# Optimization experiments

Hardware: AMD Instinct MI355X
Metric: run time of the kernel (lower is better)

Reference implementation:

```python
import jax, jax.numpy as jnp
import numpy as np
import math

D_MODEL = 1024
N_HEADS = 16
HEAD_DIM = 64


def setup_inputs() -> dict:
    key = jax.random.key(0)
    k_x, k_q, k_k, k_v, k_o = jax.random.split(key, 5)
    lecun = jax.nn.initializers.lecun_normal()
    return {
        "x": jax.random.normal(k_x, (4, 2048, D_MODEL), dtype=jnp.float32),
        "W_q": lecun(k_q, (N_HEADS, D_MODEL, HEAD_DIM), jnp.float32),
        "W_k": lecun(k_k, (N_HEADS, D_MODEL, HEAD_DIM), jnp.float32),
        "W_v": lecun(k_v, (N_HEADS, D_MODEL, HEAD_DIM), jnp.float32),
        "W_o": lecun(k_o, (D_MODEL, D_MODEL), jnp.float32),
    }


def reference(x, W_q, W_k, W_v, W_o):
    # x: [b, l, e]; W_{q,k,v}: [h, e, d]; W_o: [e, e]
    q = jnp.einsum('ble,hed->bhld', x, W_q)
    k = jnp.einsum('ble,hed->bhld', x, W_k)
    v = jnp.einsum('ble,hed->bhld', x, W_v)
    scores = jnp.einsum('bhld,bhsd->bhls', q, k) / math.sqrt(HEAD_DIM)
    attn = jax.nn.softmax(scores, axis=-1)
    av = jnp.einsum('bhls,bhsd->bhld', attn, v)  # [b, h, l, d]
    b, h, l, d = av.shape
    concat = jnp.transpose(av, (0, 2, 1, 3)).reshape(b, l, h * d)
    out = jnp.einsum('ble,eo->blo', concat, W_o)
    return jnp.asarray(out, dtype=jnp.float32)
```

## Files before the change

### kernel.cpp

```cpp
#include <hip/hip_runtime.h>

#define BATCH 4
#define LSEQ  2048
#define DM    1024
#define NH    16
#define HD    64
#define NTOK  (BATCH * LSEQ)

typedef _Float16 f16x8 __attribute__((ext_vector_type(8)));
typedef _Float16 f16x4 __attribute__((ext_vector_type(4)));
typedef __fp16   hf16x2 __attribute__((ext_vector_type(2)));
typedef float    f32x4 __attribute__((ext_vector_type(4)));

typedef __attribute__((address_space(1))) const unsigned int GU32;
typedef __attribute__((address_space(3))) unsigned int LU32;

__device__ __forceinline__ void gload_lds16(const _Float16* g, _Float16* l)
{
    __builtin_amdgcn_global_load_lds(
        (GU32*)(unsigned long long)g,
        (LU32*)(unsigned int)(unsigned long long)l, 16, 0, 0);
}


__global__ __launch_bounds__(256) void cvt_kernel(const float* __restrict__ src,
                                                  _Float16* __restrict__ dst, int n4)
{
    int i = blockIdx.x * 256 + threadIdx.x;
    if (i >= n4) return;
    float4 v = ((const float4*)src)[i];
    f16x4 h;
    h[0] = (_Float16)v.x; h[1] = (_Float16)v.y; h[2] = (_Float16)v.z; h[3] = (_Float16)v.w;
    ((f16x4*)dst)[i] = h;
}

__global__ __launch_bounds__(256) void tconv3_kernel(
    const float* __restrict__ Wq, const float* __restrict__ Wk,
    const float* __restrict__ Wv, _Float16* __restrict__ dst)
{
    const int z = blockIdx.z;
    const int which = z >> 4, h = z & 15;
    const float* __restrict__ src =
        ((which == 0) ? Wq : (which == 1) ? Wk : Wv) + (size_t)h * DM * HD;
    _Float16* __restrict__ d = dst + (size_t)z * DM * HD;
    const int e0 = blockIdx.y * 64;
    __shared__ float Ls[64][65];
    const int t = threadIdx.x;
    #pragma unroll
    for (int j = 0; j < 4; ++j) {
        int cidx = t + j * 256;
        int row = cidx >> 4, col4 = (cidx & 15) * 4;
        float4 v = *(const float4*)&src[(size_t)(e0 + row) * HD + col4];
        Ls[row][col4] = v.x; Ls[row][col4+1] = v.y; Ls[row][col4+2] = v.z; Ls[row][col4+3] = v.w;
    }
    __syncthreads();
    const int dd = t & 63, sc = t >> 6;
    alignas(16) _Float16 tmp[16];
    #pragma unroll
    for (int i = 0; i < 16; ++i) tmp[i] = (_Float16)Ls[sc * 16 + i][dd];
    *(f16x8*)&d[(size_t)dd * DM + e0 + sc * 16]     = *(f16x8*)&tmp[0];
    *(f16x8*)&d[(size_t)dd * DM + e0 + sc * 16 + 8] = *(f16x8*)&tmp[8];
}

__global__ __launch_bounds__(256) void tconv_kernel(const float* __restrict__ src,
                                                    _Float16* __restrict__ dst, int E, int D)
{
    const int d0 = blockIdx.x * 64, e0 = blockIdx.y * 64;
    __shared__ float Ls[64][65];
    const int t = threadIdx.x;
    #pragma unroll
    for (int j = 0; j < 4; ++j) {
        int cidx = t + j * 256;
        int row = cidx >> 4, col4 = (cidx & 15) * 4;
        float4 v = *(const float4*)&src[(size_t)(e0 + row) * D + d0 + col4];
        Ls[row][col4] = v.x; Ls[row][col4+1] = v.y; Ls[row][col4+2] = v.z; Ls[row][col4+3] = v.w;
    }
    __syncthreads();
    const int dd = t & 63, sc = t >> 6;
    alignas(16) _Float16 tmp[16];
    #pragma unroll
    for (int i = 0; i < 16; ++i) tmp[i] = (_Float16)Ls[sc * 16 + i][dd];
    *(f16x8*)&dst[(size_t)(d0 + dd) * E + e0 + sc * 16]     = *(f16x8*)&tmp[0];
    *(f16x8*)&dst[(size_t)(d0 + dd) * E + e0 + sc * 16 + 8] = *(f16x8*)&tmp[8];
}

template<int MODE>
__global__ __launch_bounds__(256) void gemm_kernel(
    const _Float16* __restrict__ A, const _Float16* __restrict__ B,
    float* __restrict__ out32,
    _Float16* __restrict__ qo, _Float16* __restrict__ ko, _Float16* __restrict__ vto)
{
    const int n0 = blockIdx.x * 128, m0 = blockIdx.y * 128;
    __shared__ _Float16 As[128 * 64];
    __shared__ _Float16 Bs[128 * 64];
    const int t = threadIdx.x;
    const int lane = t & 63, w = t >> 6;
    const int quad = lane >> 4, c = lane & 15;
    const int wm = (w & 1) * 64, wn = (w >> 1) * 64;
    const int srow = lane >> 3;
    const int scol8 = ((lane & 7) ^ (lane >> 3)) * 8;

    const int colsw = (quad ^ (c & 7)) * 8;
    const _Float16* Ap0 = &As[(wm + c) * 64 + colsw];
    const _Float16* Ap1 = &As[(wm + c) * 64 + (colsw ^ 32)];
    const _Float16* Bp0 = &Bs[(wn + c) * 64 + colsw];
    const _Float16* Bp1 = &Bs[(wn + c) * 64 + (colsw ^ 32)];

    f32x4 acc[4][4];
    #pragma unroll
    for (int i = 0; i < 4; ++i)
        #pragma unroll
        for (int j = 0; j < 4; ++j) acc[i][j] = {0.f, 0.f, 0.f, 0.f};

    for (int e0 = 0; e0 < DM; e0 += 64) {
        __syncthreads();
        #pragma unroll
        for (int j = 0; j < 4; ++j) {
            int ch = w * 4 + j;
            gload_lds16(A + (size_t)(m0 + ch * 8 + srow) * DM + e0 + scol8, As + ch * 512);
            gload_lds16(B + (size_t)(n0 + ch * 8 + srow) * DM + e0 + scol8, Bs + ch * 512);
        }
        __syncthreads();
        #pragma unroll
        for (int kc = 0; kc < 2; ++kc) {
            const _Float16* Ap = kc ? Ap1 : Ap0;
            const _Float16* Bp = kc ? Bp1 : Bp0;
            f16x8 af[4], bf[4];
            #pragma unroll
            for (int mt = 0; mt < 4; ++mt) af[mt] = *(const f16x8*)(Ap + mt * 1024);
            #pragma unroll
            for (int nt = 0; nt < 4; ++nt) bf[nt] = *(const f16x8*)(Bp + nt * 1024);
            #pragma unroll
            for (int mt = 0; mt < 4; ++mt)
                #pragma unroll
                for (int nt = 0; nt < 4; ++nt)
                    acc[mt][nt] = __builtin_amdgcn_mfma_f32_16x16x32_f16(af[mt], bf[nt], acc[mt][nt], 0, 0, 0);
        }
    }

    if (MODE == 0) {
        #pragma unroll
        for (int mt = 0; mt < 4; ++mt)
            #pragma unroll
            for (int nt = 0; nt < 4; ++nt)
                #pragma unroll
                for (int r = 0; r < 4; ++r) {
                    int row = m0 + wm + mt * 16 + quad * 4 + r;
                    int col = n0 + wn + nt * 16 + c;
                    out32[(size_t)row * DM + col] = acc[mt][nt][r];
                }
    } else {
        const int mi = (n0 + wn) >> 6;
        const int which = mi >> 4, hh = mi & 15;
        if (which == 2) {
            #pragma unroll
            for (int mt = 0; mt < 4; ++mt) {
                int tok0 = m0 + wm + mt * 16 + quad * 4;
                int b = tok0 >> 11, l = tok0 & (LSEQ - 1);
                #pragma unroll
                for (int nt = 0; nt < 4; ++nt) {
                    int d = nt * 16 + c;
                    f16x4 pk;
                    pk[0] = (_Float16)acc[mt][nt][0];
                    pk[1] = (_Float16)acc[mt][nt][1];
                    pk[2] = (_Float16)acc[mt][nt][2];
                    pk[3] = (_Float16)acc[mt][nt][3];
                    *(f16x4*)&vto[((size_t)(b * NH + hh) * HD + d) * LSEQ + l] = pk;
                }
            }
        } else {
            _Float16* dst = (which == 0) ? qo : ko;
            const float vs = (which == 0) ? 0.18033688011112042f : 1.0f;
            #pragma unroll
            for (int mt = 0; mt < 4; ++mt)
                #pragma unroll
                for (int nt = 0; nt < 4; ++nt)
                    #pragma unroll
                    for (int r = 0; r < 4; ++r) {
                        int tok = m0 + wm + mt * 16 + quad * 4 + r;
                        int b = tok >> 11, l = tok & (LSEQ - 1);
                        int d = nt * 16 + c;
                        dst[((size_t)(b * NH + hh) * LSEQ + l) * HD + d] = (_Float16)(acc[mt][nt][r] * vs);
                    }
        }
    }
}

__global__ __launch_bounds__(256, 4) void attn_kernel(
    const _Float16* __restrict__ Qg, const _Float16* __restrict__ Kg,
    const _Float16* __restrict__ Vtg, _Float16* __restrict__ concat)
{
    const int bh = blockIdx.x;
    const int q0 = blockIdx.y * 128;
    const int b = bh >> 4, h = bh & (NH - 1);
    __shared__ _Float16 Ks[64 * 64];
    __shared__ _Float16 Vts[64 * 64];
    __shared__ _Float16 Ps[4][32][72];
    const int t = threadIdx.x;
    const int lane = t & 63, w = t >> 6;
    const int quad = lane >> 4, c = lane & 15;
    const int srow = lane >> 3;
    const int scol8 = ((lane & 7) ^ (lane >> 3)) * 8;

    const int colsw = (quad ^ (c & 7)) * 8;
    const _Float16* Kp0 = &Ks[c * 64 + colsw];
    const _Float16* Kp1 = &Ks[c * 64 + (colsw ^ 32)];
    const _Float16* Vp0 = &Vts[c * 64 + colsw];
    const _Float16* Vp1 = &Vts[c * 64 + (colsw ^ 32)];
    _Float16*       PsW = &Ps[w][c][quad * 4];
    const _Float16* PsR = &Ps[w][c][quad * 8];

    f16x8 qf[2][2];
    #pragma unroll
    for (int mi = 0; mi < 2; ++mi)
        #pragma unroll
        for (int kc = 0; kc < 2; ++kc)
            qf[mi][kc] = *(const f16x8*)&Qg[((size_t)bh * LSEQ + q0 + w * 32 + mi * 16 + c) * HD + kc * 32 + quad * 8];

    f32x4 o[2][4];
    #pragma unroll
    for (int mi = 0; mi < 2; ++mi)
        #pragma unroll
        for (int dt = 0; dt < 4; ++dt) o[mi][dt] = {0.f, 0.f, 0.f, 0.f};
    float lp[2] = {0.f, 0.f};

    for (int s0 = 0; s0 < LSEQ; s0 += 64) {
        __syncthreads();
        #pragma unroll
        for (int j = 0; j < 2; ++j) {
            int ch = w * 2 + j;
            gload_lds16(Kg  + ((size_t)bh * LSEQ + s0 + ch * 8 + srow) * HD + scol8, Ks  + ch * 512);
            gload_lds16(Vtg + ((size_t)bh * HD + ch * 8 + srow) * LSEQ + s0 + scol8, Vts + ch * 512);
        }
        __syncthreads();

        #pragma unroll
        for (int st = 0; st < 4; ++st) {
            f32x4 sT[2];
            #pragma unroll
            for (int mi = 0; mi < 2; ++mi) sT[mi] = {0.f, 0.f, 0.f, 0.f};
            #pragma unroll
            for (int kc = 0; kc < 2; ++kc) {
                f16x8 kf = *(const f16x8*)((kc ? Kp1 : Kp0) + st * 1024);
                #pragma unroll
                for (int mi = 0; mi < 2; ++mi)
                    sT[mi] = __builtin_amdgcn_mfma_f32_16x16x32_f16(kf, qf[mi][kc], sT[mi], 0, 0, 0);
            }
            #pragma unroll
            for (int mi = 0; mi < 2; ++mi) {
                float p0 = __builtin_amdgcn_exp2f(sT[mi][0]);
                float p1 = __builtin_amdgcn_exp2f(sT[mi][1]);
                float p2 = __builtin_amdgcn_exp2f(sT[mi][2]);
                float p3 = __builtin_amdgcn_exp2f(sT[mi][3]);
                lp[mi] += (p0 + p1) + (p2 + p3);
                union { hf16x2 h2[2]; f16x4 h4; } u;
                u.h2[0] = __builtin_amdgcn_cvt_pkrtz(p0, p1);
                u.h2[1] = __builtin_amdgcn_cvt_pkrtz(p2, p3);
                *(f16x4*)(PsW + mi * 1152 + st * 16) = u.h4;
            }
        }

        #pragma unroll
        for (int sc = 0; sc < 2; ++sc) {
            f16x8 pf[2];
            #pragma unroll
            for (int mi = 0; mi < 2; ++mi)
                pf[mi] = *(const f16x8*)(PsR + mi * 1152 + sc * 32);
            #pragma unroll
            for (int dt = 0; dt < 4; ++dt) {
                f16x8 vf = *(const f16x8*)((sc ? Vp1 : Vp0) + dt * 1024);
                #pragma unroll
                for (int mi = 0; mi < 2; ++mi)
                    o[mi][dt] = __builtin_amdgcn_mfma_f32_16x16x32_f16(pf[mi], vf, o[mi][dt], 0, 0, 0);
            }
        }
    }

    #pragma unroll
    for (int mi = 0; mi < 2; ++mi) {
        lp[mi] += __shfl_xor(lp[mi], 16);
        lp[mi] += __shfl_xor(lp[mi], 32);
    }

    #pragma unroll
    for (int mi = 0; mi < 2; ++mi)
        #pragma unroll
        for (int r = 0; r < 4; ++r) {
            float inv = 1.f / __shfl(lp[mi], quad * 4 + r);
            int row = q0 + w * 32 + mi * 16 + quad * 4 + r;
            #pragma unroll
            for (int dt = 0; dt < 4; ++dt)
                concat[((size_t)b * LSEQ + row) * DM + h * HD + dt * 16 + c] =
                    (_Float16)(o[mi][dt][r] * inv);
        }
}

extern "C" void kernel_launch(void* const* d_in, const int* in_sizes, int n_in,
                              void* d_out, int out_size, void* d_ws, size_t ws_size,
                              hipStream_t stream)
{
    (void)in_sizes; (void)n_in; (void)out_size; (void)ws_size;

    const float* x  = (const float*)d_in[0];
    const float* Wq = (const float*)d_in[1];
    const float* Wk = (const float*)d_in[2];
    const float* Wv = (const float*)d_in[3];
    const float* Wo = (const float*)d_in[4];
    float* out = (float*)d_out;

    const size_t XE = (size_t)NTOK * DM;
    const size_t WQKV = (size_t)3 * NH * HD * DM;
    _Float16* xh  = (_Float16*)d_ws;
    _Float16* WtA = xh + XE;
    _Float16* Wot = WtA + WQKV;
    _Float16* q   = Wot + (size_t)DM * DM;
    _Float16* k   = q + XE;
    _Float16* vt  = k + XE;
    _Float16* cc  = vt + XE;

    cvt_kernel<<<8192, 256, 0, stream>>>(x, xh, (int)(XE / 4));
    tconv3_kernel<<<dim3(1, 16, 48), 256, 0, stream>>>(Wq, Wk, Wv, WtA);
    tconv_kernel<<<dim3(16, 16, 1), 256, 0, stream>>>(Wo, Wot, DM, DM);

    gemm_kernel<1><<<dim3(24, 64), 256, 0, stream>>>(xh, WtA, nullptr, q, k, vt);
    attn_kernel<<<dim3(64, LSEQ / 128), 256, 0, stream>>>(q, k, vt, cc);
    gemm_kernel<0><<<dim3(8, 64), 256, 0, stream>>>(cc, Wot, out, nullptr, nullptr, nullptr);
}
```

Baseline: 275.2 us.

## Double-buffer K/V tiles in attention kernel with async LDS prefetch

Gives K and V^T two LDS buffers and issues the global-to-LDS loads for the next 64-key tile before computing the current one. Explicit vmcnt waits and raw barriers replace the two __syncthreads per iteration, so load latency can overlap with the MFMA and softmax work. This doubles K/V shared memory, and launch bounds drop from 4 to 3 blocks per SIMD, which may reduce occupancy.

```diff
diff --git a/kernel.cpp b/kernel.cpp
--- a/kernel.cpp
+++ b/kernel.cpp
@@ -186,15 +186,15 @@
     }
 }
 
-__global__ __launch_bounds__(256, 4) void attn_kernel(
+__global__ __launch_bounds__(256, 3) void attn_kernel(
     const _Float16* __restrict__ Qg, const _Float16* __restrict__ Kg,
     const _Float16* __restrict__ Vtg, _Float16* __restrict__ concat)
 {
     const int bh = blockIdx.x;
     const int q0 = blockIdx.y * 128;
     const int b = bh >> 4, h = bh & (NH - 1);
-    __shared__ _Float16 Ks[64 * 64];
-    __shared__ _Float16 Vts[64 * 64];
+    __shared__ _Float16 Ks[2][64 * 64];
+    __shared__ _Float16 Vts[2][64 * 64];
     __shared__ _Float16 Ps[4][32][72];
     const int t = threadIdx.x;
     const int lane = t & 63, w = t >> 6;
@@ -203,10 +203,8 @@
     const int scol8 = ((lane & 7) ^ (lane >> 3)) * 8;
 
     const int colsw = (quad ^ (c & 7)) * 8;
-    const _Float16* Kp0 = &Ks[c * 64 + colsw];
-    const _Float16* Kp1 = &Ks[c * 64 + (colsw ^ 32)];
-    const _Float16* Vp0 = &Vts[c * 64 + colsw];
-    const _Float16* Vp1 = &Vts[c * 64 + (colsw ^ 32)];
+    const int kOffA = c * 64 + colsw;
+    const int kOffB = c * 64 + (colsw ^ 32);
     _Float16*       PsW = &Ps[w][c][quad * 4];
     const _Float16* PsR = &Ps[w][c][quad * 8];
 
@@ -224,15 +222,31 @@
         for (int dt = 0; dt < 4; ++dt) o[mi][dt] = {0.f, 0.f, 0.f, 0.f};
     float lp[2] = {0.f, 0.f};
 
-    for (int s0 = 0; s0 < LSEQ; s0 += 64) {
-        __syncthreads();
+    auto stage = [&](int bi, int s0n) {
         #pragma unroll
         for (int j = 0; j < 2; ++j) {
             int ch = w * 2 + j;
-            gload_lds16(Kg  + ((size_t)bh * LSEQ + s0 + ch * 8 + srow) * HD + scol8, Ks  + ch * 512);
-            gload_lds16(Vtg + ((size_t)bh * HD + ch * 8 + srow) * LSEQ + s0 + scol8, Vts + ch * 512);
-        }
-        __syncthreads();
+            gload_lds16(Kg  + ((size_t)bh * LSEQ + s0n + ch * 8 + srow) * HD + scol8, &Ks[bi][ch * 512]);
+            gload_lds16(Vtg + ((size_t)bh * HD + ch * 8 + srow) * LSEQ + s0n + scol8, &Vts[bi][ch * 512]);
+        }
+    };
+
+    constexpr int NT = LSEQ / 64;
+    stage(0, 0);
+    int cur = 0;
+
+    for (int tt = 0; tt < NT; ++tt) {
+        if (tt + 1 < NT) {
+            stage(cur ^ 1, (tt + 1) * 64);
+            asm volatile("s_waitcnt vmcnt(4)" ::: "memory");
+        } else {
+            asm volatile("s_waitcnt vmcnt(0)" ::: "memory");
+        }
+        __builtin_amdgcn_s_barrier();
+        __builtin_amdgcn_sched_barrier(0);
+
+        const _Float16* Kb = &Ks[cur][0];
+        const _Float16* Vb = &Vts[cur][0];
 
         #pragma unroll
         for (int st = 0; st < 4; ++st) {
@@ -241,7 +255,7 @@
             for (int mi = 0; mi < 2; ++mi) sT[mi] = {0.f, 0.f, 0.f, 0.f};
             #pragma unroll
             for (int kc = 0; kc < 2; ++kc) {
-                f16x8 kf = *(const f16x8*)((kc ? Kp1 : Kp0) + st * 1024);
+                f16x8 kf = *(const f16x8*)(Kb + (kc ? kOffB : kOffA) + st * 1024);
                 #pragma unroll
                 for (int mi = 0; mi < 2; ++mi)
                     sT[mi] = __builtin_amdgcn_mfma_f32_16x16x32_f16(kf, qf[mi][kc], sT[mi], 0, 0, 0);
@@ -268,12 +282,15 @@
                 pf[mi] = *(const f16x8*)(PsR + mi * 1152 + sc * 32);
             #pragma unroll
             for (int dt = 0; dt < 4; ++dt) {
-                f16x8 vf = *(const f16x8*)((sc ? Vp1 : Vp0) + dt * 1024);
+                f16x8 vf = *(const f16x8*)(Vb + (sc ? kOffB : kOffA) + dt * 1024);
                 #pragma unroll
                 for (int mi = 0; mi < 2; ++mi)
                     o[mi][dt] = __builtin_amdgcn_mfma_f32_16x16x32_f16(pf[mi], vf, o[mi][dt], 0, 0, 0);
             }
         }
+
+        __builtin_amdgcn_s_barrier();
+        cur ^= 1;
     }
 
     #pragma unroll
```

After: 280.2 us. Within noise of the previous version (+1.8%).
